# Optimization experiments

Hardware: AMD Instinct MI355X
Metric: run time of the kernel (lower is better)

The kernel has to match this reference:

```python
import jax, jax.numpy as jnp
import numpy as np

B, S, HID, NH, DH = 2, 1024, 4096, 32, 128
ACT_BITS, W_BITS = 8, 4
NEG_INF = float(np.finfo(np.float32).min)


def _qdq(x, bits):
    """Symmetric fake-quant over the last axis (per-token / per-out-channel), with STE."""
    qmax = 2.0 ** (bits - 1) - 1
    s = jnp.maximum(jnp.max(jnp.abs(x), axis=-1, keepdims=True) / qmax, 1e-8)
    q = jnp.clip(jnp.round(x / s), -qmax - 1, qmax) * s
    return x + jax.lax.stop_gradient(q - x)


def _rope_tables(seq_len, dim):
    inv_freq = 1.0 / (10000.0 ** (np.arange(0, dim, 2, dtype=np.float32) / dim))
    t = np.arange(seq_len, dtype=np.float32)
    freqs = np.outer(t, inv_freq)              # [S, DH/2]
    emb = np.concatenate([freqs, freqs], -1)   # [S, DH]
    return jnp.asarray(np.cos(emb)), jnp.asarray(np.sin(emb))


def _rotate_half(x):
    h = x.shape[-1] // 2
    return jnp.concatenate([-x[..., h:], x[..., :h]], axis=-1)


def _norm(x):
    return jnp.linalg.norm(x, axis=-1, keepdims=True)


def setup_inputs() -> dict:
    key = jax.random.key(0)
    ks = jax.random.split(key, 5)
    causal = jnp.where(jnp.tril(jnp.ones((S, S), dtype=bool)), 0.0, NEG_INF).astype(jnp.float32)
    return {
        "hidden_states": jax.random.normal(ks[0], (B, S, HID), jnp.float32),
        "wq": jax.random.normal(ks[1], (HID, HID), jnp.float32) * 0.02,
        "wk": jax.random.normal(ks[2], (HID, HID), jnp.float32) * 0.02,
        "wv": jax.random.normal(ks[3], (HID, HID), jnp.float32) * 0.02,
        "wo": jax.random.normal(ks[4], (HID, HID), jnp.float32) * 0.02,
        "attention_mask": jnp.broadcast_to(causal[None, None], (B, 1, S, S)),
    }


def reference(hidden_states, wq, wk, wv, wo, attention_mask):
    cos, sin = _rope_tables(S, DH)
    cos, sin = cos[None, None], sin[None, None]          # [1,1,S,DH]
    x = _qdq(hidden_states, ACT_BITS)                    # act fake-quant (per token)

    def proj(w):
        return jnp.einsum('bsh,dh->bsd', x, _qdq(w, W_BITS)).reshape(B, S, NH, DH).transpose(0, 2, 1, 3)

    q, k, v = proj(wq), proj(wk), proj(wv)               # [B,H,S,D]
    q = q * cos + _rotate_half(q) * sin
    k = k * cos + _rotate_half(k) * sin

    # qkt_matmul: quant Q and K, rescale scores by quantization norm ratios a1, a2
    x1len = _norm(q)
    qq = _qdq(q, ACT_BITS)
    a1 = _norm(qq) / x1len                               # [B,H,S,1]
    x2len = _norm(k)
    kq = _qdq(k, ACT_BITS)
    a2 = jnp.swapaxes(_norm(kq) / x2len, 2, 3)           # [B,H,1,S]

    attn = jnp.einsum('bhqd,bhkd->bhqk', qq, kq) / np.float32(np.sqrt(DH))
    attn = attn / a1 / a2
    attn = attn + attention_mask
    attn = jnp.maximum(attn, NEG_INF)
    p = jax.nn.softmax(attn.astype(jnp.float32), axis=-1)

    # pv_matmul: quant P and V, rescale output by V's norm ratio
    pq = _qdq(p, ACT_BITS)
    x2len_v = _norm(v)
    vq = _qdq(v, ACT_BITS)
    a2v = _norm(vq) / x2len_v                            # [B,H,S,1]

    out = jnp.einsum('bhqk,bhkd->bhqd', pq, vq) / a2v    # [B,H,S,D]
    out = out.transpose(0, 2, 1, 3).reshape(B, S, HID)
    out = jnp.einsum('bsh,dh->bsd', _qdq(out, ACT_BITS), _qdq(wo, W_BITS))
    return out
```

## Files before the change

### kernel.cpp

```cpp
#include <hip/hip_runtime.h>
#include <hip/hip_bf16.h>
#include <math.h>
#include <stdint.h>

#define NEG_INF_F (-3.4028234663852886e38f)

typedef __bf16 bf16_t;
typedef __bf16 bf16x8 __attribute__((ext_vector_type(8)));
typedef float f32x4 __attribute__((ext_vector_type(4)));
typedef float f32x16 __attribute__((ext_vector_type(16)));
typedef int i32x4 __attribute__((ext_vector_type(4)));
typedef int i32x16 __attribute__((ext_vector_type(16)));
typedef int8_t c8x4 __attribute__((ext_vector_type(4)));

static constexpr int Bb = 2, Ss = 1024, Hid = 4096, Nh = 32, Dh = 128;
static constexpr int Mr = Bb * Ss;
static constexpr int Bh = Bb * Nh;

__device__ __forceinline__ void gload_lds16(const void* g, void* l) {
  __builtin_amdgcn_global_load_lds((const __attribute__((address_space(1))) void*)g,
                                   (__attribute__((address_space(3))) void*)l, 16, 0, 0);
}

__device__ __forceinline__ float wred_max(float v) {
#pragma unroll
  for (int off = 32; off > 0; off >>= 1) v = fmaxf(v, __shfl_xor(v, off));
  return v;
}

__device__ __forceinline__ unsigned pkbf(float a, float b) {
  unsigned short ua = __builtin_bit_cast(unsigned short, (bf16_t)a);
  unsigned short ub = __builtin_bit_cast(unsigned short, (bf16_t)b);
  return (unsigned)ua | ((unsigned)ub << 16);
}

__global__ void rope_table_kernel(float* __restrict__ ctab, float* __restrict__ stab) {
  int i = blockIdx.x * 256 + threadIdx.x;
  int srow = i >> 6, d = i & 63;
  float invf = (float)pow(10000.0, -((double)(2 * d) / (double)Dh));
  float ang = (float)srow * invf;
  ctab[i] = (float)cos((double)ang);
  stab[i] = (float)sin((double)ang);
}

__device__ __forceinline__ void quant_row_body(
    const float* __restrict__ x, int8_t* __restrict__ o, float* __restrict__ scale,
    int row, int ncols, float qmax, float clo, float chi)
{
  const int tid = threadIdx.x;
  const float4* x4 = (const float4*)x;
  const int n4 = ncols >> 2;
  float m = 0.f;
  for (int i = tid; i < n4; i += 256) {
    float4 v = x4[i];
    m = fmaxf(m, fmaxf(fmaxf(fabsf(v.x), fabsf(v.y)), fmaxf(fabsf(v.z), fabsf(v.w))));
  }
  m = wred_max(m);
  __shared__ float red[4];
  if ((tid & 63) == 0) red[tid >> 6] = m;
  __syncthreads();
  m = fmaxf(fmaxf(red[0], red[1]), fmaxf(red[2], red[3]));
  const float s = fmaxf(m / qmax, 1e-8f);
  if (tid == 0) scale[row] = s;
  c8x4* o4 = (c8x4*)o;
  for (int i = tid; i < n4; i += 256) {
    float4 v = x4[i];
    c8x4 r;
    r[0] = (int8_t)(int)fminf(fmaxf(rintf(v.x / s), clo), chi);
    r[1] = (int8_t)(int)fminf(fmaxf(rintf(v.y / s), clo), chi);
    r[2] = (int8_t)(int)fminf(fmaxf(rintf(v.z / s), clo), chi);
    r[3] = (int8_t)(int)fminf(fmaxf(rintf(v.w / s), clo), chi);
    o4[i] = r;
  }
}

__global__ __launch_bounds__(256) void quant_rows_kernel(
    const float* __restrict__ in, int8_t* __restrict__ outq,
    float* __restrict__ scale, int ncols, float qmax, float clo, float chi)
{
  const int row = blockIdx.x;
  quant_row_body(in + (size_t)row * ncols, outq + (size_t)row * ncols, scale,
                 row, ncols, qmax, clo, chi);
}

__global__ __launch_bounds__(256) void quant_w3_kernel(
    const float* __restrict__ w0, const float* __restrict__ w1, const float* __restrict__ w2,
    int8_t* __restrict__ o0, int8_t* __restrict__ o1, int8_t* __restrict__ o2,
    float* __restrict__ s0, float* __restrict__ s1, float* __restrict__ s2)
{
  const int sel = blockIdx.x >> 12, row = blockIdx.x & 4095;
  const float* in = sel == 0 ? w0 : (sel == 1 ? w1 : w2);
  int8_t* o = sel == 0 ? o0 : (sel == 1 ? o1 : o2);
  float* sc = sel == 0 ? s0 : (sel == 1 ? s1 : s2);
  quant_row_body(in + (size_t)row * Hid, o + (size_t)row * Hid, sc, row, Hid,
                 7.f, -8.f, 7.f);
}

#define GEMM_WAITBAR(N)                                                               \
  asm volatile("s_waitcnt vmcnt(" #N ")" ::: "memory");                               \
  __builtin_amdgcn_sched_barrier(0);                                                  \
  __builtin_amdgcn_s_barrier();                                                       \
  __builtin_amdgcn_sched_barrier(0);

#define GEMM_BARONLY                                                                  \
  __builtin_amdgcn_sched_barrier(0);                                                  \
  __builtin_amdgcn_s_barrier();                                                       \
  __builtin_amdgcn_sched_barrier(0);

#define GEMM_STAGE128(koff, Abuf, Bbuf)                                               \
  _Pragma("unroll")                                                                   \
  for (int r = 0; r < 4; ++r) {                                                       \
    gload_lds16(gA + (koff) + (size_t)r * 32 * K, (Abuf) + r * 4096 + wid * 1024);    \
    gload_lds16(gB + (koff) + (size_t)r * 32 * K, (Bbuf) + r * 4096 + wid * 1024);    \
  }

#define GEMM_PHASE128(Abuf, Bbuf)                                                     \
  _Pragma("unroll")                                                                   \
  for (int g = 0; g < 2; ++g) {                                                       \
    i32x4 af[4], bw[4];                                                               \
    _Pragma("unroll")                                                                 \
    for (int f = 0; f < 4; ++f) {                                                     \
      const int ca = (((g << 2) | kg4) ^ (l15 & 7)) * 16;                             \
      af[f] = *(const i32x4*)&(Abuf)[(wm * 64 + f * 16 + l15) * 128 + ca];            \
      bw[f] = *(const i32x4*)&(Bbuf)[(f * 32 + wn * 16 + l15) * 128 + ca];            \
    }                                                                                 \
    _Pragma("unroll")                                                                 \
    for (int fm = 0; fm < 4; ++fm)                                                    \
      _Pragma("unroll")                                                               \
      for (int fn = 0; fn < 4; ++fn)                                                  \
        acc[fm][fn] = __builtin_amdgcn_mfma_i32_16x16x64_i8(af[fm], bw[fn],           \
                                                            acc[fm][fn], 0, 0, 0);   \
  }

#define GEMM_CORE_PIPE(SMEM)                                                          \
  int8_t* A0 = (int8_t*)(SMEM);                                                       \
  int8_t* A1 = (int8_t*)(SMEM) + 16384;                                               \
  int8_t* B0 = (int8_t*)(SMEM) + 32768;                                               \
  int8_t* B1 = (int8_t*)(SMEM) + 49152;                                               \
  const int strow = wid * 8 + (lane >> 3);                                            \
  const int schunk = ((lane & 7) ^ (lane >> 3)) * 16;                                 \
  const int8_t* gA = A + (size_t)(bm + strow) * K + schunk;                           \
  const int8_t* gB = W + (size_t)(bn + strow) * K + schunk;                           \
  i32x4 acc[4][4] = {};                                                               \
  GEMM_STAGE128(0, A0, B0)                                                            \
  GEMM_STAGE128(128, A1, B1)                                                          \
  for (int k0 = 0; k0 + 512 <= K; k0 += 256) {                                        \
    GEMM_WAITBAR(8)                                                                   \
    GEMM_PHASE128(A0, B0)                                                             \
    GEMM_BARONLY                                                                      \
    GEMM_STAGE128(k0 + 256, A0, B0)                                                   \
    GEMM_WAITBAR(8)                                                                   \
    GEMM_PHASE128(A1, B1)                                                             \
    GEMM_BARONLY                                                                      \
    GEMM_STAGE128(k0 + 384, A1, B1)                                                   \
  }                                                                                   \
  GEMM_WAITBAR(8)                                                                     \
  GEMM_PHASE128(A0, B0)                                                               \
  GEMM_BARONLY                                                                        \
  GEMM_WAITBAR(0)                                                                     \
  GEMM_PHASE128(A1, B1)

__global__ __launch_bounds__(256) void qkv_gemm_kernel(
    const int8_t* __restrict__ A, const float* __restrict__ sA,
    const int8_t* __restrict__ wqz, const int8_t* __restrict__ wkz, const int8_t* __restrict__ wvz,
    const float* __restrict__ swq, const float* __restrict__ swk, const float* __restrict__ swv,
    int8_t* __restrict__ qqb, float* __restrict__ Fq,
    int8_t* __restrict__ kqb, float* __restrict__ Fk,
    bf16_t* __restrict__ vdq, float* __restrict__ a2vp,
    const float* __restrict__ ctab, const float* __restrict__ stab)
{
  __shared__ __align__(16) char smem[65536 + 3072];
  float (*s_red)[128][3] = (float (*)[128][3])(smem + 65536);

  const int tid = threadIdx.x, lane = tid & 63, wid = tid >> 6;
  const int id = blockIdx.x;
  const int xcd = id & 7, within = id >> 3;
  const int nIdx = xcd * 12 + (within >> 4);
  const int mIdx = within & 15;
  const int wsel = nIdx >> 5, head = nIdx & 31;
  const int bm = mIdx * 128, bn = head * 128;
  const int8_t* W = wsel == 0 ? wqz : (wsel == 1 ? wkz : wvz);
  const float* sW = wsel == 0 ? swq : (wsel == 1 ? swk : swv);
  constexpr int K = Hid;

  const int wm = wid >> 1, wn = wid & 1;
  const int l15 = lane & 15, kg4 = lane >> 4;

  GEMM_CORE_PIPE(smem)

  float sav[4][4], swv_[4];
#pragma unroll
  for (int fm = 0; fm < 4; ++fm)
#pragma unroll
    for (int j = 0; j < 4; ++j) sav[fm][j] = sA[bm + wm * 64 + fm * 16 + kg4 * 4 + j];
#pragma unroll
  for (int fn = 0; fn < 4; ++fn) swv_[fn] = sW[bn + fn * 32 + wn * 16 + l15];

  float val[4][4][4];
#pragma unroll
  for (int fm = 0; fm < 4; ++fm)
#pragma unroll
    for (int fn = 0; fn < 4; ++fn)
#pragma unroll
      for (int j = 0; j < 4; ++j)
        val[fm][fn][j] = (float)acc[fm][fn][j] * sav[fm][j] * swv_[fn];

  const int b = bm >> 10;
  const int bh = b * Nh + head;
  float r_[4][4][4];
  if (wsel != 2) {
    const int dmA = wn * 16 + l15, dmB = 32 + wn * 16 + l15;
#pragma unroll
    for (int fm = 0; fm < 4; ++fm)
#pragma unroll
      for (int j = 0; j < 4; ++j) {
        const int srow = (bm + wm * 64 + fm * 16 + kg4 * 4 + j) & (Ss - 1);
        const float cA = ctab[srow * 64 + dmA], cB = ctab[srow * 64 + dmB];
        const float sA_ = stab[srow * 64 + dmA], sB_ = stab[srow * 64 + dmB];
        r_[fm][0][j] = __fsub_rn(__fmul_rn(val[fm][0][j], cA), __fmul_rn(val[fm][2][j], sA_));
        r_[fm][1][j] = __fsub_rn(__fmul_rn(val[fm][1][j], cB), __fmul_rn(val[fm][3][j], sB_));
        r_[fm][2][j] = __fadd_rn(__fmul_rn(val[fm][2][j], cA), __fmul_rn(val[fm][0][j], sA_));
        r_[fm][3][j] = __fadd_rn(__fmul_rn(val[fm][3][j], cB), __fmul_rn(val[fm][1][j], sB_));
      }
  } else {
#pragma unroll
    for (int fm = 0; fm < 4; ++fm)
#pragma unroll
      for (int fn = 0; fn < 4; ++fn)
#pragma unroll
        for (int j = 0; j < 4; ++j) r_[fm][fn][j] = val[fm][fn][j];
  }
  float ma_[4][4], n2_[4][4];
#pragma unroll
  for (int fm = 0; fm < 4; ++fm)
#pragma unroll
    for (int j = 0; j < 4; ++j) {
      float ma = 0.f, n2 = 0.f;
#pragma unroll
      for (int fn = 0; fn < 4; ++fn) {
        const float x = r_[fm][fn][j];
        ma = fmaxf(ma, fabsf(x));
        n2 += x * x;
      }
#pragma unroll
      for (int off = 1; off < 16; off <<= 1) {
        ma = fmaxf(ma, __shfl_xor(ma, off));
        n2 += __shfl_xor(n2, off);
      }
      ma_[fm][j] = ma;
      n2_[fm][j] = n2;
    }
  if (l15 == 0) {
#pragma unroll
    for (int fm = 0; fm < 4; ++fm)
#pragma unroll
      for (int j = 0; j < 4; ++j) {
        const int rl = wm * 64 + fm * 16 + kg4 * 4 + j;
        s_red[wn][rl][0] = ma_[fm][j];
        s_red[wn][rl][1] = n2_[fm][j];
      }
  }
  __syncthreads();
  float qc[4][4][4], svl[4][4], n2c[4][4], nq2_[4][4];
#pragma unroll
  for (int fm = 0; fm < 4; ++fm)
#pragma unroll
    for (int j = 0; j < 4; ++j) {
      const int rl = wm * 64 + fm * 16 + kg4 * 4 + j;
      const float ma = fmaxf(ma_[fm][j], s_red[wn ^ 1][rl][0]);
      const float n2 = n2_[fm][j] + s_red[wn ^ 1][rl][1];
      const float s = fmaxf(ma / 127.0f, 1e-8f);
      float nq2 = 0.f;
#pragma unroll
      for (int fn = 0; fn < 4; ++fn) {
        const float q = fminf(fmaxf(rintf(r_[fm][fn][j] / s), -128.f), 127.f);
        qc[fm][fn][j] = q;
        nq2 += q * q;
      }
#pragma unroll
      for (int off = 1; off < 16; off <<= 1) nq2 += __shfl_xor(nq2, off);
      svl[fm][j] = s;
      n2c[fm][j] = n2;
      nq2_[fm][j] = nq2;
    }
  __syncthreads();
  if (l15 == 0) {
#pragma unroll
    for (int fm = 0; fm < 4; ++fm)
#pragma unroll
      for (int j = 0; j < 4; ++j)
        s_red[wn][wm * 64 + fm * 16 + kg4 * 4 + j][2] = nq2_[fm][j];
  }
  __syncthreads();

  if (wsel != 2) {
    int8_t* outq = (wsel == 0) ? qqb : kqb;
    float* Ff = (wsel == 0) ? Fq : Fk;
#pragma unroll
    for (int fm = 0; fm < 4; ++fm)
#pragma unroll
      for (int j = 0; j < 4; ++j) {
        const int rl = wm * 64 + fm * 16 + kg4 * 4 + j;
        const int stok = (bm + rl) & (Ss - 1);
        const size_t rowBase = ((size_t)bh * Ss + stok) * Dh;
#pragma unroll
        for (int fn = 0; fn < 4; ++fn)
          outq[rowBase + fn * 32 + wn * 16 + l15] = (int8_t)(int)qc[fm][fn][j];
        if (wn == 0 && l15 == 0) {
          const float nq2 = nq2_[fm][j] + s_red[1][rl][2];
          Ff[(size_t)bh * Ss + stok] = sqrtf(n2c[fm][j] / nq2) * 0.2973017787506803f;
        }
      }
  } else {
    bf16_t* svt = (bf16_t*)smem;
#pragma unroll
    for (int fm = 0; fm < 4; ++fm)
#pragma unroll
      for (int j = 0; j < 4; ++j) {
        const int t = wm * 64 + fm * 16 + kg4 * 4 + j;
#pragma unroll
        for (int fn = 0; fn < 4; ++fn) {
          const int d = fn * 32 + wn * 16 + l15;
          svt[d * 136 + t] = (bf16_t)(qc[fm][fn][j] * svl[fm][j]);
        }
        if (wn == 0 && l15 == 0) {
          const float nq2 = nq2_[fm][j] + s_red[1][t][2];
          a2vp[(size_t)bh * Ss + ((bm + t) & (Ss - 1))] =
              svl[fm][j] * sqrtf(nq2) / sqrtf(n2c[fm][j]);
        }
      }
    __syncthreads();
    const int d = tid >> 1, toff = (tid & 1) * 64;
    const int s0 = bm & (Ss - 1);
    const bf16_t* src = svt + d * 136 + toff;
    bf16_t* dst = vdq + ((size_t)bh * Dh + d) * Ss + s0 + toff;
#pragma unroll
    for (int k = 0; k < 8; ++k) {
      bf16x8 tv;
#pragma unroll
      for (int e = 0; e < 8; ++e) tv[e] = src[k * 8 + e];
      *(bf16x8*)(dst + k * 8) = tv;
    }
  }
}

__global__ __launch_bounds__(256) void gemm0_kernel(
    const int8_t* __restrict__ A, const float* __restrict__ sA,
    const int8_t* __restrict__ W, const float* __restrict__ sW,
    float* __restrict__ out, int M, int N, int K)
{
  __shared__ __align__(16) char smem[65536];
  const int tid = threadIdx.x, lane = tid & 63, wid = tid >> 6;
  const int id = blockIdx.x;
  const int xcd = id & 7, within = id >> 3;
  const int nIdx = xcd * 4 + (within >> 4);
  const int mIdx = within & 15;
  const int bm = mIdx * 128, bn = nIdx * 128;
  const int wm = wid >> 1, wn = wid & 1;
  const int l15 = lane & 15, kg4 = lane >> 4;

  GEMM_CORE_PIPE(smem)

#pragma unroll
  for (int fm = 0; fm < 4; ++fm) {
#pragma unroll
    for (int j = 0; j < 4; ++j) {
      const int row = bm + wm * 64 + fm * 16 + kg4 * 4 + j;
      const float sa = sA[row];
#pragma unroll
      for (int fn = 0; fn < 4; ++fn) {
        const int col = bn + fn * 32 + wn * 16 + l15;
        out[(size_t)row * N + col] = (float)acc[fm][fn][j] * sa * sW[col];
      }
    }
  }
}

#define KR(r) (((r) & 3) + 8 * ((r) >> 2) + 4 * hi)
__global__ __launch_bounds__(64, 2) void attn_kernel(
    const int8_t* __restrict__ qq, const int8_t* __restrict__ kq,
    const bf16_t* __restrict__ vdqt,
    const float* __restrict__ Fq, const float* __restrict__ Fk,
    const float* __restrict__ A2v, float* __restrict__ oattn)
{
  const int bh = blockIdx.x, b = bh >> 5, h = bh & 31;
  const int lane = threadIdx.x & 63;
  const int l31 = lane & 31, hi = lane >> 5;
  const int u = 31 - (int)blockIdx.y;
  const int q0 = u * 32;
  const int nt = u + 1;
  const size_t bhS = (size_t)bh * Ss;

  const int8_t* qrow = qq + (bhS + q0 + l31) * Dh + hi * 16;
  i32x4 qf[4];
#pragma unroll
  for (int c = 0; c < 4; ++c) qf[c] = *(const i32x4*)(qrow + c * 32);
  const float fq = Fq[bhS + q0 + l31];
  const int qcol = q0 + l31;

  float m = NEG_INF_F;
  int t = 0;
  for (; t + 1 < nt; t += 2) {
    const int kb0 = t * 32, kb1 = kb0 + 32;
    const int8_t* kr0 = kq + (bhS + kb0 + l31) * Dh + hi * 16;
    const int8_t* kr1 = kq + (bhS + kb1 + l31) * Dh + hi * 16;
    i32x16 ca = {}, cb = {}, da = {}, db = {};
    ca = __builtin_amdgcn_mfma_i32_32x32x32_i8(*(const i32x4*)(kr0),      qf[0], ca, 0, 0, 0);
    cb = __builtin_amdgcn_mfma_i32_32x32x32_i8(*(const i32x4*)(kr0 + 64), qf[2], cb, 0, 0, 0);
    da = __builtin_amdgcn_mfma_i32_32x32x32_i8(*(const i32x4*)(kr1),      qf[0], da, 0, 0, 0);
    db = __builtin_amdgcn_mfma_i32_32x32x32_i8(*(const i32x4*)(kr1 + 64), qf[2], db, 0, 0, 0);
    ca = __builtin_amdgcn_mfma_i32_32x32x32_i8(*(const i32x4*)(kr0 + 32), qf[1], ca, 0, 0, 0);
    cb = __builtin_amdgcn_mfma_i32_32x32x32_i8(*(const i32x4*)(kr0 + 96), qf[3], cb, 0, 0, 0);
    da = __builtin_amdgcn_mfma_i32_32x32x32_i8(*(const i32x4*)(kr1 + 32), qf[1], da, 0, 0, 0);
    db = __builtin_amdgcn_mfma_i32_32x32x32_i8(*(const i32x4*)(kr1 + 96), qf[3], db, 0, 0, 0);
    float4 fk40[4], fk41[4];
#pragma unroll
    for (int g = 0; g < 4; ++g) fk40[g] = *(const float4*)&Fk[bhS + kb0 + g * 8 + 4 * hi];
#pragma unroll
    for (int g = 0; g < 4; ++g) fk41[g] = *(const float4*)&Fk[bhS + kb1 + g * 8 + 4 * hi];
    const bool diag1 = (t + 1 == nt - 1);
#pragma unroll
    for (int r = 0; r < 16; ++r) {
      m = fmaxf(m, (float)(ca[r] + cb[r]) * fq * ((const float*)&fk40[r >> 2])[r & 3]);
      const float v1 = (float)(da[r] + db[r]) * fq * ((const float*)&fk41[r >> 2])[r & 3];
      if (!diag1 || (kb1 + KR(r) <= qcol)) m = fmaxf(m, v1);
    }
  }
  if (t < nt) {
    const int kb = t * 32;
    const int8_t* krow = kq + (bhS + kb + l31) * Dh + hi * 16;
    i32x16 ca = {}, cb = {};
    ca = __builtin_amdgcn_mfma_i32_32x32x32_i8(*(const i32x4*)(krow),      qf[0], ca, 0, 0, 0);
    cb = __builtin_amdgcn_mfma_i32_32x32x32_i8(*(const i32x4*)(krow + 64), qf[2], cb, 0, 0, 0);
    ca = __builtin_amdgcn_mfma_i32_32x32x32_i8(*(const i32x4*)(krow + 32), qf[1], ca, 0, 0, 0);
    cb = __builtin_amdgcn_mfma_i32_32x32x32_i8(*(const i32x4*)(krow + 96), qf[3], cb, 0, 0, 0);
    float4 fk4[4];
#pragma unroll
    for (int g = 0; g < 4; ++g) fk4[g] = *(const float4*)&Fk[bhS + kb + g * 8 + 4 * hi];
#pragma unroll
    for (int r = 0; r < 16; ++r) {
      const float v = (float)(ca[r] + cb[r]) * fq * ((const float*)&fk4[r >> 2])[r & 3];
      if (kb + KR(r) <= qcol) m = fmaxf(m, v);
    }
  }
  m = fmaxf(m, __shfl_xor(m, 32));

  float z = 0.f;
  f32x16 oacc[4] = {};
  for (int tt = 0; tt < nt; ++tt) {
    const int kb = tt * 32;
    const int8_t* krow = kq + (bhS + kb + l31) * Dh + hi * 16;
    i32x16 ca = {}, cb = {};
    ca = __builtin_amdgcn_mfma_i32_32x32x32_i8(*(const i32x4*)(krow),      qf[0], ca, 0, 0, 0);
    cb = __builtin_amdgcn_mfma_i32_32x32x32_i8(*(const i32x4*)(krow + 64), qf[2], cb, 0, 0, 0);
    ca = __builtin_amdgcn_mfma_i32_32x32x32_i8(*(const i32x4*)(krow + 32), qf[1], ca, 0, 0, 0);
    cb = __builtin_amdgcn_mfma_i32_32x32x32_i8(*(const i32x4*)(krow + 96), qf[3], cb, 0, 0, 0);
    float4 fk4[4];
#pragma unroll
    for (int g = 0; g < 4; ++g) fk4[g] = *(const float4*)&Fk[bhS + kb + g * 8 + 4 * hi];
    float p[16];
    const bool diag = (tt == nt - 1);
#pragma unroll
    for (int r = 0; r < 16; ++r) {
      float v = (float)(ca[r] + cb[r]) * fq * ((const float*)&fk4[r >> 2])[r & 3];
      if (diag && (kb + KR(r) > qcol)) v = NEG_INF_F;
      const float e = __expf(v - m);
      z += e;
      p[r] = rintf(127.0f * e);
    }
#pragma unroll
    for (int s = 0; s < 2; ++s) {
      const int rs = s * 8;
      unsigned k0 = pkbf(p[rs + 0], p[rs + 1]);
      unsigned k1 = pkbf(p[rs + 2], p[rs + 3]);
      unsigned k2 = pkbf(p[rs + 4], p[rs + 5]);
      unsigned k3 = pkbf(p[rs + 6], p[rs + 7]);
      unsigned sx0 = __shfl_xor(k0, 32);
      unsigned sx1 = __shfl_xor(k1, 32);
      unsigned sx2 = __shfl_xor(k2, 32);
      unsigned sx3 = __shfl_xor(k3, 32);
      uint4 ww;
      ww.x = hi ? sx2 : k0;
      ww.y = hi ? sx3 : k1;
      ww.z = hi ? k2 : sx0;
      ww.w = hi ? k3 : sx1;
      const bf16x8 af = __builtin_bit_cast(bf16x8, ww);
      const int kg2 = kb + s * 16 + hi * 8;
#pragma unroll
      for (int dt = 0; dt < 4; ++dt) {
        const bf16x8 vf = *(const bf16x8*)(vdqt + ((size_t)bh * Dh + dt * 32 + l31) * Ss + kg2);
        oacc[dt] = __builtin_amdgcn_mfma_f32_32x32x16_bf16(af, vf, oacc[dt], 0, 0, 0);
      }
    }
  }
  z += __shfl_xor(z, 32);
  const float osc = (1.0f / z) / 127.0f / A2v[bhS + q0 + l31];
#pragma unroll
  for (int dt = 0; dt < 4; ++dt) {
#pragma unroll
    for (int r = 0; r < 16; ++r) {
      const int q = q0 + KR(r);
      const float oscr = __shfl(osc, KR(r));
      oattn[((size_t)b * Ss + q) * Hid + h * Dh + dt * 32 + l31] = oacc[dt][r] * oscr;
    }
  }
}

extern "C" void kernel_launch(void* const* d_in, const int* in_sizes, int n_in,
                              void* d_out, int out_size, void* d_ws, size_t ws_size,
                              hipStream_t stream)
{
  const float* hidden = (const float*)d_in[0];
  const float* wq = (const float*)d_in[1];
  const float* wk = (const float*)d_in[2];
  const float* wv = (const float*)d_in[3];
  const float* wo = (const float*)d_in[4];
  float* out = (float*)d_out;

  char* p = (char*)d_ws;
  auto alloc = [&](size_t bytes) -> char* {
    char* r = p; p += (bytes + 255) & ~(size_t)255; return r;
  };
  int8_t* xq   = (int8_t*)alloc((size_t)Mr * Hid);
  int8_t* wb0  = (int8_t*)alloc((size_t)Hid * Hid);
  int8_t* wb1  = (int8_t*)alloc((size_t)Hid * Hid);
  int8_t* wb2  = (int8_t*)alloc((size_t)Hid * Hid);
  float*  oat  = (float*) alloc((size_t)Bh * Ss * Dh * sizeof(float));
  int8_t* qqb  = (int8_t*)alloc((size_t)Bh * Ss * Dh);
  int8_t* kqb  = (int8_t*)alloc((size_t)Bh * Ss * Dh);
  bf16_t* vdqt = (bf16_t*)alloc((size_t)Bh * Dh * Ss * sizeof(bf16_t));
  float* sxa = (float*)alloc((size_t)Mr * sizeof(float));
  float* sw0 = (float*)alloc((size_t)Hid * sizeof(float));
  float* sw1 = (float*)alloc((size_t)Hid * sizeof(float));
  float* sw2 = (float*)alloc((size_t)Hid * sizeof(float));
  float* Fq  = (float*)alloc((size_t)Bh * Ss * sizeof(float));
  float* Fk  = (float*)alloc((size_t)Bh * Ss * sizeof(float));
  float* A2v = (float*)alloc((size_t)Bh * Ss * sizeof(float));
  float* soa = (float*)alloc((size_t)Mr * sizeof(float));
  float* ctab = (float*)alloc((size_t)Ss * 64 * sizeof(float));
  float* stab = (float*)alloc((size_t)Ss * 64 * sizeof(float));
  int8_t* oq  = xq;

  rope_table_kernel<<<Ss * 64 / 256, 256, 0, stream>>>(ctab, stab);
  quant_rows_kernel<<<Mr, 256, 0, stream>>>(hidden, xq, sxa, Hid, 127.f, -128.f, 127.f);
  quant_w3_kernel<<<3 * Hid, 256, 0, stream>>>(wq, wk, wv, wb0, wb1, wb2, sw0, sw1, sw2);

  qkv_gemm_kernel<<<1536, 256, 0, stream>>>(xq, sxa, wb0, wb1, wb2, sw0, sw1, sw2,
                                            qqb, Fq, kqb, Fk, vdqt, A2v, ctab, stab);

  dim3 ga(Bh, 32);
  attn_kernel<<<ga, 64, 0, stream>>>(qqb, kqb, vdqt, Fq, Fk, A2v, oat);

  quant_rows_kernel<<<Mr, 256, 0, stream>>>(oat, oq, soa, Hid, 127.f, -128.f, 127.f);
  quant_rows_kernel<<<Hid, 256, 0, stream>>>(wo, wb0, sw0, Hid, 7.f, -8.f, 7.f);
  gemm0_kernel<<<512, 256, 0, stream>>>(oq, soa, wb0, sw0, out, Mr, Hid, Hid);
}
```

Measured before the change: 373.3 us.

## Merge wo quantization into batched weight quant and simplify output GEMM

The wo weight quantization moves into the batched weight-quant kernel, which now handles four matrices, so one launch does the work of two. The output-projection GEMM no longer uses the shared pipelined core macro. It is replaced with a simple single-buffered loop: global-to-LDS loads, a barrier, then int8 MFMA over two k-groups. This drops the software pipelining, so load latency may be exposed in the output GEMM in exchange for removing a launch.

```diff
diff --git a/kernel.cpp b/kernel.cpp
--- a/kernel.cpp
+++ b/kernel.cpp
@@ -83,15 +83,18 @@
                  row, ncols, qmax, clo, chi);
 }
 
-__global__ __launch_bounds__(256) void quant_w3_kernel(
-    const float* __restrict__ w0, const float* __restrict__ w1, const float* __restrict__ w2,
-    int8_t* __restrict__ o0, int8_t* __restrict__ o1, int8_t* __restrict__ o2,
-    float* __restrict__ s0, float* __restrict__ s1, float* __restrict__ s2)
+__global__ __launch_bounds__(256) void quant_w4_kernel(
+    const float* __restrict__ w0, const float* __restrict__ w1,
+    const float* __restrict__ w2, const float* __restrict__ w3,
+    int8_t* __restrict__ o0, int8_t* __restrict__ o1,
+    int8_t* __restrict__ o2, int8_t* __restrict__ o3,
+    float* __restrict__ s0, float* __restrict__ s1,
+    float* __restrict__ s2, float* __restrict__ s3)
 {
   const int sel = blockIdx.x >> 12, row = blockIdx.x & 4095;
-  const float* in = sel == 0 ? w0 : (sel == 1 ? w1 : w2);
-  int8_t* o = sel == 0 ? o0 : (sel == 1 ? o1 : o2);
-  float* sc = sel == 0 ? s0 : (sel == 1 ? s1 : s2);
+  const float* in = sel == 0 ? w0 : (sel == 1 ? w1 : (sel == 2 ? w2 : w3));
+  int8_t* o = sel == 0 ? o0 : (sel == 1 ? o1 : (sel == 2 ? o2 : o3));
+  float* sc = sel == 0 ? s0 : (sel == 1 ? s1 : (sel == 2 ? s2 : s3));
   quant_row_body(in + (size_t)row * Hid, o + (size_t)row * Hid, sc, row, Hid,
                  7.f, -8.f, 7.f);
 }
@@ -349,7 +352,8 @@
     const int8_t* __restrict__ W, const float* __restrict__ sW,
     float* __restrict__ out, int M, int N, int K)
 {
-  __shared__ __align__(16) char smem[65536];
+  __shared__ __align__(16) int8_t As[128 * 128];
+  __shared__ __align__(16) int8_t Bs[128 * 128];
   const int tid = threadIdx.x, lane = tid & 63, wid = tid >> 6;
   const int id = blockIdx.x;
   const int xcd = id & 7, within = id >> 3;
@@ -359,8 +363,36 @@
   const int wm = wid >> 1, wn = wid & 1;
   const int l15 = lane & 15, kg4 = lane >> 4;
 
-  GEMM_CORE_PIPE(smem)
-
+  const int strow = wid * 8 + (lane >> 3);
+  const int schunk = ((lane & 7) ^ (lane >> 3)) * 16;
+  const int8_t* gA = A + (size_t)(bm + strow) * K + schunk;
+  const int8_t* gB = W + (size_t)(bn + strow) * K + schunk;
+
+  i32x4 acc[4][4] = {};
+  for (int k0 = 0; k0 < K; k0 += 128) {
+    if (k0) __syncthreads();
+#pragma unroll
+    for (int r = 0; r < 4; ++r) {
+      gload_lds16(gA + k0 + (size_t)r * 32 * K, As + r * 4096 + wid * 1024);
+      gload_lds16(gB + k0 + (size_t)r * 32 * K, Bs + r * 4096 + wid * 1024);
+    }
+    __syncthreads();
+#pragma unroll
+    for (int g = 0; g < 2; ++g) {
+      i32x4 af[4], bw[4];
+#pragma unroll
+      for (int f = 0; f < 4; ++f) {
+        const int ca = (((g << 2) | kg4) ^ (l15 & 7)) * 16;
+        af[f] = *(const i32x4*)&As[(wm * 64 + f * 16 + l15) * 128 + ca];
+        bw[f] = *(const i32x4*)&Bs[(f * 32 + wn * 16 + l15) * 128 + ca];
+      }
+#pragma unroll
+      for (int fm = 0; fm < 4; ++fm)
+#pragma unroll
+        for (int fn = 0; fn < 4; ++fn)
+          acc[fm][fn] = __builtin_amdgcn_mfma_i32_16x16x64_i8(af[fm], bw[fn], acc[fm][fn], 0, 0, 0);
+    }
+  }
 #pragma unroll
   for (int fm = 0; fm < 4; ++fm) {
 #pragma unroll
@@ -525,6 +557,7 @@
   int8_t* wb0  = (int8_t*)alloc((size_t)Hid * Hid);
   int8_t* wb1  = (int8_t*)alloc((size_t)Hid * Hid);
   int8_t* wb2  = (int8_t*)alloc((size_t)Hid * Hid);
+  int8_t* wb3  = (int8_t*)alloc((size_t)Hid * Hid);
   float*  oat  = (float*) alloc((size_t)Bh * Ss * Dh * sizeof(float));
   int8_t* qqb  = (int8_t*)alloc((size_t)Bh * Ss * Dh);
   int8_t* kqb  = (int8_t*)alloc((size_t)Bh * Ss * Dh);
@@ -533,6 +566,7 @@
   float* sw0 = (float*)alloc((size_t)Hid * sizeof(float));
   float* sw1 = (float*)alloc((size_t)Hid * sizeof(float));
   float* sw2 = (float*)alloc((size_t)Hid * sizeof(float));
+  float* sw3 = (float*)alloc((size_t)Hid * sizeof(float));
   float* Fq  = (float*)alloc((size_t)Bh * Ss * sizeof(float));
   float* Fk  = (float*)alloc((size_t)Bh * Ss * sizeof(float));
   float* A2v = (float*)alloc((size_t)Bh * Ss * sizeof(float));
@@ -543,7 +577,8 @@
 
   rope_table_kernel<<<Ss * 64 / 256, 256, 0, stream>>>(ctab, stab);
   quant_rows_kernel<<<Mr, 256, 0, stream>>>(hidden, xq, sxa, Hid, 127.f, -128.f, 127.f);
-  quant_w3_kernel<<<3 * Hid, 256, 0, stream>>>(wq, wk, wv, wb0, wb1, wb2, sw0, sw1, sw2);
+  quant_w4_kernel<<<4 * Hid, 256, 0, stream>>>(wq, wk, wv, wo, wb0, wb1, wb2, wb3,
+                                               sw0, sw1, sw2, sw3);
 
   qkv_gemm_kernel<<<1536, 256, 0, stream>>>(xq, sxa, wb0, wb1, wb2, sw0, sw1, sw2,
                                             qqb, Fq, kqb, Fk, vdqt, A2v, ctab, stab);
@@ -552,6 +587,5 @@
   attn_kernel<<<ga, 64, 0, stream>>>(qqb, kqb, vdqt, Fq, Fk, A2v, oat);
 
   quant_rows_kernel<<<Mr, 256, 0, stream>>>(oat, oq, soa, Hid, 127.f, -128.f, 127.f);
-  quant_rows_kernel<<<Hid, 256, 0, stream>>>(wo, wb0, sw0, Hid, 7.f, -8.f, 7.f);
-  gemm0_kernel<<<512, 256, 0, stream>>>(oq, soa, wb0, sw0, out, Mr, Hid, Hid);
-}
+  gemm0_kernel<<<512, 256, 0, stream>>>(oq, soa, wb3, sw3, out, Mr, Hid, Hid);
+}
```

New measurement: 373.1 us. Within noise of the previous version (-0.1%).
